# Kernel tuning notes

Measured on AMD Instinct MI355X. Metric: run time of the kernel, lower is better.

The kernel has to match this reference:

```python
import jax, jax.numpy as jnp
import numpy as np

N, C, G = 50000, 30, 1000   # cells, classes, genes
E = 800000                   # edges
OUT = 8                      # GATv2 out channels, heads=1


def setup_inputs() -> dict:
    key = jax.random.key(0)
    ks = jax.random.split(key, 12)
    X = jax.random.normal(ks[0], (N, G), dtype=jnp.float32)
    Mu = jax.random.normal(ks[1], (C, G), dtype=jnp.float32)
    Var = jax.random.uniform(ks[2], (C, G), dtype=jnp.float32) + 0.5  # strictly positive
    edge_index = jax.random.randint(ks[3], (2, E), 0, N, dtype=jnp.int64)
    # learned params
    W = 0.01 * jax.random.normal(ks[4], (N, C), dtype=jnp.float32)   # torch init zeros; small noise for nontrivial P
    S = jnp.ones((N, 1), dtype=jnp.float32)
    sc = 1.0 / np.sqrt(G)
    Wl = sc * jax.random.normal(ks[5], (OUT, G), dtype=jnp.float32)  # lin_l weight
    bl = jnp.zeros((OUT,), dtype=jnp.float32)
    Wr = sc * jax.random.normal(ks[6], (OUT, G), dtype=jnp.float32)  # lin_r weight
    br = jnp.zeros((OUT,), dtype=jnp.float32)
    att = jax.random.normal(ks[7], (OUT,), dtype=jnp.float32) / np.sqrt(OUT)
    return {"X": X, "Mu": Mu, "Var": Var, "edge_index": edge_index,
            "W": W, "S": S, "Wl": Wl, "bl": bl, "Wr": Wr, "br": br, "att": att}


def reference(X, Mu, Var, edge_index, W, S, Wl, bl, Wr, br, att):
    n = X.shape[0]
    P = jax.nn.softmax(W, axis=1)                       # [N,C]
    # Gaussian log-likelihood term. Expand (X - Mu*S)^2/Var summed over genes:
    invVar = 1.0 / Var                                  # [C,G]
    A = (X * X) @ invVar.T                              # [N,C]  sum X^2/Var
    B = X @ (Mu * invVar).T                             # [N,C]  sum X*Mu/Var
    D = jnp.sum(Mu * Mu * invVar, axis=1)               # [C]    sum Mu^2/Var
    Fmat = -0.5 * (A - 2.0 * S * B + (S * S) * D[None, :])  # [N,C]
    ll_prot = jnp.sum(P * Fmat) / n

    # GATv2 attention (heads=1, add_self_loops=False)
    x_l = X @ Wl.T + bl                                 # [N,8] source transform
    x_r = X @ Wr.T + br                                 # [N,8] target transform
    src, dst = edge_index[0], edge_index[1]
    m = jax.nn.leaky_relu(x_l[src] + x_r[dst], negative_slope=0.2)  # [E,8]
    e = m @ att                                         # [E]
    # edge-softmax grouped by destination node
    emax = jax.ops.segment_max(e, dst, num_segments=n)  # [N]
    e_exp = jnp.exp(e - emax[dst])                      # [E]
    denom = jax.ops.segment_sum(e_exp, dst, num_segments=n)  # [N]
    alpha = e_exp / (denom[dst] + 1e-16)                # [E]

    ce_space = -jnp.sum(P[src] * alpha[:, None] * jnp.log(P[dst] + 1e-8)) / n
    return ll_prot, ce_space, P
```

## Files before the change

### kernel.cpp

```cpp
#include <hip/hip_runtime.h>
#include <hip/hip_bf16.h>
#include <math.h>

#define N_CELLS 50000
#define C_CLS   30
#define G_GENES 1000
#define E_EDGES 800000
#define KPAD    1024
#define NREP    4

typedef __attribute__((ext_vector_type(8))) short bf16x8;
typedef __attribute__((ext_vector_type(4))) float f32x4;

__device__ __forceinline__ unsigned f2bf_u(float f) {
    unsigned u = __float_as_uint(f);
    return (u + 0x7fffu + ((u >> 16) & 1u)) >> 16;
}
__device__ __forceinline__ unsigned pack2(float lo, float hi) {
    union { __hip_bfloat162 h; unsigned u; } cv;
    cv.h = __float22bfloat162_rn(make_float2(lo, hi));
    return cv.u;
}
__device__ __forceinline__ float bf2f(unsigned short u) {
    return __uint_as_float(((unsigned)u) << 16);
}

__device__ __forceinline__ float lrelu02(float v) { return v > 0.f ? v : 0.2f * v; }

__device__ __forceinline__ float dp4(int4 a, int4 b) {
    const unsigned* ua = (const unsigned*)&a;
    const unsigned* ub = (const unsigned*)&b;
    float s = 0.f;
#pragma unroll
    for (int i = 0; i < 4; i++) {
        float al = __uint_as_float(ua[i] << 16);
        float ah = __uint_as_float(ua[i] & 0xffff0000u);
        float bl = __uint_as_float(ub[i] << 16);
        float bh = __uint_as_float(ub[i] & 0xffff0000u);
        s += al * bl + ah * bh;
    }
    return s;
}

__global__ void prep_kernel(const float* __restrict__ Mu, const float* __restrict__ Var,
                            const float* __restrict__ Wl, const float* __restrict__ Wr,
                            unsigned short* __restrict__ CoefB, float* __restrict__ Dvec,
                            float* __restrict__ dn4, float* __restrict__ out) {
    const int r = blockIdx.x;
    const int t = threadIdx.x;
    __shared__ float red[256];
    float dacc = 0.f;
    for (int g = t; g < KPAD; g += 256) {
        float v = 0.f;
        if (g < G_GENES) {
            if (r < 30) {
                float iv = 1.0f / Var[r * G_GENES + g];
                float mu = Mu[r * G_GENES + g];
                v = iv;
                dacc += mu * mu * iv;
            } else if (r >= 32) {
                int i = r - 32;
                if (i < 30)      v = Mu[i * G_GENES + g] / Var[i * G_GENES + g];
                else if (i < 38) v = Wl[(i - 30) * G_GENES + g];
                else if (i < 46) v = Wr[(i - 38) * G_GENES + g];
            }
        }
        CoefB[r * KPAD + g] = (unsigned short)f2bf_u(v);
    }
    for (int i = blockIdx.x * 256 + t; i < N_CELLS * NREP * 2; i += 80 * 256) dn4[i] = 0.f;
    if (r == 31 && t < 2) out[t] = 0.f;

    if (r < 30) {
        red[t] = dacc;
        __syncthreads();
        for (int s = 128; s > 0; s >>= 1) {
            if (t < s) red[t] += red[t + s];
            __syncthreads();
        }
        if (t == 0) Dvec[r] = red[0];
    }
}

__global__ __launch_bounds__(256, 4) void main_rows_kernel(
    const float* __restrict__ X, const float* __restrict__ W,
    const float* __restrict__ S, const float* __restrict__ bl,
    const float* __restrict__ br, const unsigned short* __restrict__ CoefB,
    const float* __restrict__ Dvec,
    float* __restrict__ out,
    unsigned short* __restrict__ Pb, unsigned short* __restrict__ Lb,
    float* __restrict__ xl, float* __restrict__ xr)
{
    __shared__ __align__(16) unsigned short Ct[2][80 * 72];

    const int t    = threadIdx.x;
    const int w    = t >> 6;
    const int l    = t & 63;
    const int l15  = l & 15;
    const int quad = l >> 4;
    const int k0q  = quad * 8;
    const int wavebase = blockIdx.x * 64 + w * 16;
    const bool valid = (wavebase < N_CELLS);
    const float* __restrict__ xrow = X + (size_t)(wavebase + l15) * G_GENES;

    const int srow = t >> 3;
    const int scol = (t & 7) << 3;
    const bool s3  = (t < 128);
    const unsigned short* __restrict__ cb0 = &CoefB[srow * KPAD + scol];

    f32x4 acc[5];
#pragma unroll
    for (int i = 0; i < 5; i++) acc[i] = (f32x4){0.f, 0.f, 0.f, 0.f};

    {
        int4 p0 = *(const int4*)(cb0);
        int4 p1 = *(const int4*)(cb0 + 32 * KPAD);
        *(int4*)&Ct[0][srow * 72 + scol] = p0;
        *(int4*)&Ct[0][(srow + 32) * 72 + scol] = p1;
        if (s3) {
            int4 p2 = *(const int4*)(cb0 + 64 * KPAD);
            *(int4*)&Ct[0][(srow + 64) * 72 + scol] = p2;
        }
    }

    float4 c0a = make_float4(0.f, 0.f, 0.f, 0.f), c0b = c0a, c1a = c0a, c1b = c0a;
    if (valid) {
        c0a = *(const float4*)&xrow[k0q];
        c0b = *(const float4*)&xrow[k0q + 4];
        c1a = *(const float4*)&xrow[32 + k0q];
        c1b = *(const float4*)&xrow[32 + k0q + 4];
    }
    __syncthreads();

#pragma unroll 2
    for (int kt = 0; kt < KPAD; kt += 64) {
        const int cur = (kt >> 6) & 1;
        const int ktn = kt + 64;

        int4 q0, q1, q2;
        if (ktn < KPAD) {
            q0 = *(const int4*)(cb0 + ktn);
            q1 = *(const int4*)(cb0 + 32 * KPAD + ktn);
            if (s3) q2 = *(const int4*)(cb0 + 64 * KPAD + ktn);
        }

        float4 n0a = make_float4(0.f, 0.f, 0.f, 0.f), n0b = n0a, n1a = n0a, n1b = n0a;
        if (valid && ktn < KPAD) {
            const int ka = ktn + k0q;
            n0a = *(const float4*)&xrow[ka];
            n0b = *(const float4*)&xrow[ka + 4];
            const int kb = ktn + 32 + k0q;
            if (kb < G_GENES) {
                n1a = *(const float4*)&xrow[kb];
                n1b = *(const float4*)&xrow[kb + 4];
            }
        }

        union { unsigned u[4]; bf16x8 v; } ua, u2;
        ua.u[0] = pack2(c0a.x, c0a.y); ua.u[1] = pack2(c0a.z, c0a.w);
        ua.u[2] = pack2(c0b.x, c0b.y); ua.u[3] = pack2(c0b.z, c0b.w);
        u2.u[0] = pack2(c0a.x * c0a.x, c0a.y * c0a.y);
        u2.u[1] = pack2(c0a.z * c0a.z, c0a.w * c0a.w);
        u2.u[2] = pack2(c0b.x * c0b.x, c0b.y * c0b.y);
        u2.u[3] = pack2(c0b.z * c0b.z, c0b.w * c0b.w);
#pragma unroll
        for (int nt = 0; nt < 5; nt++) {
            bf16x8 b = *(const bf16x8*)&Ct[cur][(nt * 16 + l15) * 72 + k0q];
            acc[nt] = __builtin_amdgcn_mfma_f32_16x16x32_bf16(
                nt < 2 ? u2.v : ua.v, b, acc[nt], 0, 0, 0);
        }
        ua.u[0] = pack2(c1a.x, c1a.y); ua.u[1] = pack2(c1a.z, c1a.w);
        ua.u[2] = pack2(c1b.x, c1b.y); ua.u[3] = pack2(c1b.z, c1b.w);
        u2.u[0] = pack2(c1a.x * c1a.x, c1a.y * c1a.y);
        u2.u[1] = pack2(c1a.z * c1a.z, c1a.w * c1a.w);
        u2.u[2] = pack2(c1b.x * c1b.x, c1b.y * c1b.y);
        u2.u[3] = pack2(c1b.z * c1b.z, c1b.w * c1b.w);
#pragma unroll
        for (int nt = 0; nt < 5; nt++) {
            bf16x8 b = *(const bf16x8*)&Ct[cur][(nt * 16 + l15) * 72 + 32 + k0q];
            acc[nt] = __builtin_amdgcn_mfma_f32_16x16x32_bf16(
                nt < 2 ? u2.v : ua.v, b, acc[nt], 0, 0, 0);
        }

        if (ktn < KPAD) {
            *(int4*)&Ct[cur ^ 1][srow * 72 + scol] = q0;
            *(int4*)&Ct[cur ^ 1][(srow + 32) * 72 + scol] = q1;
            if (s3) *(int4*)&Ct[cur ^ 1][(srow + 64) * 72 + scol] = q2;
            __syncthreads();
        }

        c0a = n0a; c0b = n0b; c1a = n1a; c1b = n1b;
    }

    if (!valid) return;

    const int rbase = wavebase + quad * 4;
    const bool c2ok = (l15 < 14);
    const float d0 = Dvec[l15];
    const float d1 = c2ok ? Dvec[16 + l15] : 0.f;
    float llacc = 0.f;
#pragma unroll
    for (int r = 0; r < 4; r++) {
        const int row = rbase + r;
        float w0 = W[(size_t)row * 30 + l15];
        float w1 = c2ok ? W[(size_t)row * 30 + 16 + l15] : -1e30f;
        float m = fmaxf(w0, w1);
#pragma unroll
        for (int mm = 1; mm < 16; mm <<= 1) m = fmaxf(m, __shfl_xor(m, mm, 64));
        float e0 = __expf(w0 - m);
        float e1 = c2ok ? __expf(w1 - m) : 0.f;
        float s = e0 + e1;
#pragma unroll
        for (int mm = 1; mm < 16; mm <<= 1) s += __shfl_xor(s, mm, 64);
        float inv = 1.0f / s;
        float p0 = e0 * inv, p1 = e1 * inv;
        float Sn = S[row], Sn2 = Sn * Sn;
        float F0 = -0.5f * (acc[0][r] - 2.0f * Sn * acc[2][r] + Sn2 * d0);
        float F1 = -0.5f * (acc[1][r] - 2.0f * Sn * acc[3][r] + Sn2 * d1);
        float lp = p0 * F0 + (c2ok ? p1 * F1 : 0.f);
#pragma unroll
        for (int mm = 1; mm < 16; mm <<= 1) lp += __shfl_xor(lp, mm, 64);
        llacc += lp;

        out[2 + (size_t)row * 30 + l15] = p0;
        float lg0 = __logf(p0 + 1e-8f);
        Pb[(size_t)row * 32 + l15] = (unsigned short)f2bf_u(p0);
        Lb[(size_t)row * 32 + l15] = (unsigned short)f2bf_u(lg0);
        if (c2ok) {
            out[2 + (size_t)row * 30 + 16 + l15] = p1;
            float lg1 = __logf(p1 + 1e-8f);
            Pb[(size_t)row * 32 + 16 + l15] = (unsigned short)f2bf_u(p1);
            Lb[(size_t)row * 32 + 16 + l15] = (unsigned short)f2bf_u(lg1);
        } else {
            Pb[(size_t)row * 32 + 16 + l15] = 0;
            Lb[(size_t)row * 32 + 16 + l15] = 0;
        }
        if (l15 >= 14)                xl[(size_t)row * 8 + (l15 - 14)] = acc[3][r] + bl[l15 - 14];
        else if (l15 < 6)             xl[(size_t)row * 8 + (l15 + 2)]  = acc[4][r] + bl[l15 + 2];
        if (l15 >= 6 && l15 < 14)     xr[(size_t)row * 8 + (l15 - 6)]  = acc[4][r] + br[l15 - 6];
    }
    llacc += __shfl_xor(llacc, 16, 64);
    llacc += __shfl_xor(llacc, 32, 64);
    if (l == 0) atomicAdd(&out[0], llacc * (1.0f / N_CELLS));
}

__global__ __launch_bounds__(256) void edge_pass(
    const int* __restrict__ ei, const float* __restrict__ xl,
    const float* __restrict__ xr, const float* __restrict__ att,
    const unsigned short* __restrict__ Pb, const unsigned short* __restrict__ Lb,
    float* __restrict__ dn4) {
    const int t = threadIdx.x;
    const int g = t >> 2;
    const int j = t & 3;
    const int e = blockIdx.x * 64 + g;
    const int src = ei[e];
    const int dst = ei[E_EDGES + e];

    float2 lv = *(const float2*)&xl[(size_t)src * 8 + j * 2];
    float2 rv = *(const float2*)&xr[(size_t)dst * 8 + j * 2];
    float2 av = *(const float2*)&att[j * 2];
    float ev = lrelu02(lv.x + rv.x) * av.x + lrelu02(lv.y + rv.y) * av.y;
    ev += __shfl_xor(ev, 1, 64);
    ev += __shfl_xor(ev, 2, 64);
    float p = __expf(ev);

    int4 a = *(const int4*)&Pb[(size_t)src * 32 + j * 8];
    int4 b = *(const int4*)&Lb[(size_t)dst * 32 + j * 8];
    float dot = dp4(a, b);
    dot += __shfl_xor(dot, 1, 64);
    dot += __shfl_xor(dot, 2, 64);

    float* base = &dn4[((size_t)(blockIdx.x & (NREP - 1)) * N_CELLS + dst) * 2];
    if (j == 0)      atomicAdd(base, p);
    else if (j == 1) atomicAdd(base + 1, p * dot);
}

__global__ __launch_bounds__(256) void finalize_kernel(const float* __restrict__ dn4,
                                                       float* __restrict__ out) {
    const int t = threadIdx.x;
    const int i = blockIdx.x * 256 + t;
    float c = 0.f;
    if (i < N_CELLS) {
        float d  = (dn4[(size_t)i * 2]     + dn4[((size_t)N_CELLS + i) * 2]) +
                   (dn4[((size_t)2 * N_CELLS + i) * 2] + dn4[((size_t)3 * N_CELLS + i) * 2]);
        float nm = (dn4[(size_t)i * 2 + 1] + dn4[((size_t)N_CELLS + i) * 2 + 1]) +
                   (dn4[((size_t)2 * N_CELLS + i) * 2 + 1] + dn4[((size_t)3 * N_CELLS + i) * 2 + 1]);
        c = nm / (d + 1e-16f);
    }
#pragma unroll
    for (int m = 1; m < 64; m <<= 1) c += __shfl_xor(c, m, 64);
    __shared__ float wsum[4];
    if ((t & 63) == 0) wsum[t >> 6] = c;
    __syncthreads();
    if (t == 0)
        atomicAdd(&out[1], -(wsum[0] + wsum[1] + wsum[2] + wsum[3]) * (1.0f / N_CELLS));
}

extern "C" void kernel_launch(void* const* d_in, const int* in_sizes, int n_in,
                              void* d_out, int out_size, void* d_ws, size_t ws_size,
                              hipStream_t stream) {
    const float* X   = (const float*)d_in[0];
    const float* Mu  = (const float*)d_in[1];
    const float* Var = (const float*)d_in[2];
    const int*   ei  = (const int*)d_in[3];
    const float* W   = (const float*)d_in[4];
    const float* S   = (const float*)d_in[5];
    const float* Wl  = (const float*)d_in[6];
    const float* bl  = (const float*)d_in[7];
    const float* Wr  = (const float*)d_in[8];
    const float* br  = (const float*)d_in[9];
    const float* att = (const float*)d_in[10];

    float* out = (float*)d_out;

    float* wsf = (float*)d_ws;
    unsigned short* CoefB  = (unsigned short*)wsf;
    float* Dvec            = wsf + 40960;
    unsigned short* Pb     = (unsigned short*)(wsf + 40992);
    unsigned short* Lb     = (unsigned short*)(wsf + 840992);
    float* xl              = wsf + 1640992;
    float* xr              = wsf + 2040992;
    float* dn4             = wsf + 2440992;

    prep_kernel<<<80, 256, 0, stream>>>(Mu, Var, Wl, Wr, CoefB, Dvec, dn4, out);
    main_rows_kernel<<<(N_CELLS + 63) / 64, 256, 0, stream>>>(
        X, W, S, bl, br, CoefB, Dvec, out, Pb, Lb, xl, xr);
    edge_pass<<<E_EDGES / 64, 256, 0, stream>>>(ei, xl, xr, att, Pb, Lb, dn4);
    finalize_kernel<<<(N_CELLS + 255) / 256, 256, 0, stream>>>(dn4, out);
}
```

Before: 443.6 us.

## Deepen global prefetch to two stages and use LDS-only barrier in main GEMM loop

The main rows kernel now prefetches both X rows and the coefficient tile two K-steps ahead instead of one, holding an extra set of registers in flight. The block barrier is replaced by a custom barrier that waits only on LDS counters, so outstanding global loads need not drain before syncing. Launch bounds are lowered from 4 to 3 blocks per CU so the added registers fit, which trades occupancy for more memory-level parallelism.

```diff
diff --git a/kernel.cpp b/kernel.cpp
--- a/kernel.cpp
+++ b/kernel.cpp
@@ -26,6 +26,11 @@
 }
 
 __device__ __forceinline__ float lrelu02(float v) { return v > 0.f ? v : 0.2f * v; }
+
+__device__ __forceinline__ void lds_barrier() {
+    asm volatile("s_waitcnt lgkmcnt(0)" ::: "memory");
+    __builtin_amdgcn_s_barrier();
+}
 
 __device__ __forceinline__ float dp4(int4 a, int4 b) {
     const unsigned* ua = (const unsigned*)&a;
@@ -81,7 +86,7 @@
     }
 }
 
-__global__ __launch_bounds__(256, 4) void main_rows_kernel(
+__global__ __launch_bounds__(256, 3) void main_rows_kernel(
     const float* __restrict__ X, const float* __restrict__ W,
     const float* __restrict__ S, const float* __restrict__ bl,
     const float* __restrict__ br, const unsigned short* __restrict__ CoefB,
@@ -121,37 +126,46 @@
             *(int4*)&Ct[0][(srow + 64) * 72 + scol] = p2;
         }
     }
-
-    float4 c0a = make_float4(0.f, 0.f, 0.f, 0.f), c0b = c0a, c1a = c0a, c1b = c0a;
+    int4 qc0 = *(const int4*)(cb0 + 64);
+    int4 qc1 = *(const int4*)(cb0 + 32 * KPAD + 64);
+    int4 qc2 = make_int4(0, 0, 0, 0);
+    if (s3) qc2 = *(const int4*)(cb0 + 64 * KPAD + 64);
+
+    float4 z4 = make_float4(0.f, 0.f, 0.f, 0.f);
+    float4 c0a = z4, c0b = z4, c1a = z4, c1b = z4;
+    float4 n0a = z4, n0b = z4, n1a = z4, n1b = z4;
     if (valid) {
         c0a = *(const float4*)&xrow[k0q];
         c0b = *(const float4*)&xrow[k0q + 4];
         c1a = *(const float4*)&xrow[32 + k0q];
         c1b = *(const float4*)&xrow[32 + k0q + 4];
-    }
-    __syncthreads();
+        n0a = *(const float4*)&xrow[64 + k0q];
+        n0b = *(const float4*)&xrow[64 + k0q + 4];
+        n1a = *(const float4*)&xrow[96 + k0q];
+        n1b = *(const float4*)&xrow[96 + k0q + 4];
+    }
+    lds_barrier();
 
 #pragma unroll 2
     for (int kt = 0; kt < KPAD; kt += 64) {
         const int cur = (kt >> 6) & 1;
-        const int ktn = kt + 64;
-
-        int4 q0, q1, q2;
-        if (ktn < KPAD) {
-            q0 = *(const int4*)(cb0 + ktn);
-            q1 = *(const int4*)(cb0 + 32 * KPAD + ktn);
-            if (s3) q2 = *(const int4*)(cb0 + 64 * KPAD + ktn);
-        }
-
-        float4 n0a = make_float4(0.f, 0.f, 0.f, 0.f), n0b = n0a, n1a = n0a, n1b = n0a;
-        if (valid && ktn < KPAD) {
-            const int ka = ktn + k0q;
-            n0a = *(const float4*)&xrow[ka];
-            n0b = *(const float4*)&xrow[ka + 4];
-            const int kb = ktn + 32 + k0q;
-            if (kb < G_GENES) {
-                n1a = *(const float4*)&xrow[kb];
-                n1b = *(const float4*)&xrow[kb + 4];
+        const int kt2 = kt + 128;
+
+        int4 qn0 = make_int4(0, 0, 0, 0), qn1 = qn0, qn2 = qn0;
+        float4 m0a = z4, m0b = z4, m1a = z4, m1b = z4;
+        if (kt2 < KPAD) {
+            qn0 = *(const int4*)(cb0 + kt2);
+            qn1 = *(const int4*)(cb0 + 32 * KPAD + kt2);
+            if (s3) qn2 = *(const int4*)(cb0 + 64 * KPAD + kt2);
+            if (valid) {
+                const int ka = kt2 + k0q;
+                m0a = *(const float4*)&xrow[ka];
+                m0b = *(const float4*)&xrow[ka + 4];
+                const int kb = kt2 + 32 + k0q;
+                if (kb < G_GENES) {
+                    m1a = *(const float4*)&xrow[kb];
+                    m1b = *(const float4*)&xrow[kb + 4];
+                }
             }
         }
 
@@ -181,14 +195,16 @@
                 nt < 2 ? u2.v : ua.v, b, acc[nt], 0, 0, 0);
         }
 
-        if (ktn < KPAD) {
-            *(int4*)&Ct[cur ^ 1][srow * 72 + scol] = q0;
-            *(int4*)&Ct[cur ^ 1][(srow + 32) * 72 + scol] = q1;
-            if (s3) *(int4*)&Ct[cur ^ 1][(srow + 64) * 72 + scol] = q2;
-            __syncthreads();
+        if (kt + 64 < KPAD) {
+            *(int4*)&Ct[cur ^ 1][srow * 72 + scol] = qc0;
+            *(int4*)&Ct[cur ^ 1][(srow + 32) * 72 + scol] = qc1;
+            if (s3) *(int4*)&Ct[cur ^ 1][(srow + 64) * 72 + scol] = qc2;
+            lds_barrier();
         }
 
         c0a = n0a; c0b = n0b; c1a = n1a; c1b = n1b;
+        n0a = m0a; n0b = m0b; n1a = m1a; n1b = m1b;
+        qc0 = qn0; qc1 = qn1; qc2 = qn2;
     }
 
     if (!valid) return;
```

Measured after the change: 442.8 us. Within noise of the previous version (-0.2%).
